# Optimization experiments

Hardware: AMD Instinct MI355X
Metric: run time of the kernel (lower is better)

Reference implementation:

```python
import jax, jax.numpy as jnp
import numpy as np

N_EMBD = 384
NUM_HEADS = 6
HEAD_SIZE = 64


def setup_inputs() -> dict:
    key = jax.random.key(0)
    ks = jax.random.split(key, 6)
    B, T = 128, 256
    D = NUM_HEADS * HEAD_SIZE  # 384
    x = jax.random.normal(ks[0], (B, T, N_EMBD), dtype=jnp.float32)
    Wk = jax.random.normal(ks[1], (N_EMBD, D), dtype=jnp.float32) * (N_EMBD ** -0.5)
    Wq = jax.random.normal(ks[2], (N_EMBD, D), dtype=jnp.float32) * (N_EMBD ** -0.5)
    Wv = jax.random.normal(ks[3], (N_EMBD, D), dtype=jnp.float32) * (N_EMBD ** -0.5)
    Wp = jax.random.normal(ks[4], (D, N_EMBD), dtype=jnp.float32) * (D ** -0.5)
    bp = jax.random.normal(ks[5], (N_EMBD,), dtype=jnp.float32) * 0.01
    return {"x": x, "Wk": Wk, "Wq": Wq, "Wv": Wv, "Wp": Wp, "bp": bp}


def reference(x, Wk, Wq, Wv, Wp, bp):
    B, T, C = x.shape
    H, hs = NUM_HEADS, HEAD_SIZE
    # QKV projections -> [B, H, T, hs]
    q = (x @ Wq).reshape(B, T, H, hs).transpose(0, 2, 1, 3)
    k = (x @ Wk).reshape(B, T, H, hs).transpose(0, 2, 1, 3)
    v = (x @ Wv).reshape(B, T, H, hs).transpose(0, 2, 1, 3)
    # NOTE: original scales by C**-0.5 where C = n_embd (not head_size)
    scale = jnp.asarray(C, x.dtype) ** -0.5
    wei = jnp.einsum('bhtd,bhsd->bhts', q, k) * scale  # [B, H, T, T]
    causal = jnp.tril(jnp.ones((T, T), dtype=bool))
    wei = jnp.where(causal, wei, -jnp.inf)
    wei = jax.nn.softmax(wei, axis=-1)
    # dropout disabled (eval mode) for deterministic reference
    out = jnp.einsum('bhts,bhsd->bhtd', wei, v)  # [B, H, T, hs]
    out = out.transpose(0, 2, 1, 3).reshape(B, T, H * hs)
    return out @ Wp + bp
```

## Files before the change

### kernel.cpp

```cpp
#include <hip/hip_runtime.h>
#include <hip/hip_bf16.h>


#define T_SEQ 256
#define NH 6
#define HS 64
#define CIN 384
#define BATCH 128
#define BT (BATCH * T_SEQ)
#define ELEMS ((size_t)BT * CIN)

using f32x4  = __attribute__((ext_vector_type(4))) float;
using bf16x8 = __attribute__((ext_vector_type(8))) short;

typedef __attribute__((address_space(3))) void       lds_vp;
typedef __attribute__((address_space(1))) const void glob_vp;

static __device__ __forceinline__ unsigned short f2bf(float f) {
  union { float f; unsigned u; } v; v.f = f;
  unsigned r = v.u + 0x7FFFu + ((v.u >> 16) & 1u);
  return (unsigned short)(r >> 16);
}

static __device__ __forceinline__ bf16x8 ld_bf8(const unsigned short* p) {
  return *reinterpret_cast<const bf16x8*>(p);
}

static __device__ __forceinline__ void gl_lds16(const void* g, void* l) {
  __builtin_amdgcn_global_load_lds((glob_vp*)g, (lds_vp*)l, 16, 0, 0);
}

__global__ __launch_bounds__(256) void convert_x(
    const float* __restrict__ x, unsigned short* __restrict__ xb)
{
  size_t i = (((size_t)blockIdx.x << 8) + threadIdx.x) << 3;
  float4 f0 = *reinterpret_cast<const float4*>(x + i);
  float4 f1 = *reinterpret_cast<const float4*>(x + i + 4);
  uint4 pk;
  pk.x = f2bf(f0.x) | ((unsigned)f2bf(f0.y) << 16);
  pk.y = f2bf(f0.z) | ((unsigned)f2bf(f0.w) << 16);
  pk.z = f2bf(f1.x) | ((unsigned)f2bf(f1.y) << 16);
  pk.w = f2bf(f1.z) | ((unsigned)f2bf(f1.w) << 16);
  *reinterpret_cast<uint4*>(xb + i) = pk;
}

__global__ __launch_bounds__(256) void convert_wqkv(
    const float* __restrict__ Wq, const float* __restrict__ Wk,
    const float* __restrict__ Wv, unsigned short* __restrict__ dst)
{
  __shared__ float t[32][33];
  const int z = blockIdx.z;
  const float* __restrict__ W = (z == 0) ? Wq : (z == 1) ? Wk : Wv;
  const int tx = threadIdx.x & 31, ty = threadIdx.x >> 5;
  const int k0 = blockIdx.x * 32, n0 = blockIdx.y * 32;
#pragma unroll
  for (int i = 0; i < 4; ++i)
    t[ty + 8 * i][tx] = W[(size_t)(k0 + ty + 8 * i) * CIN + n0 + tx];
  __syncthreads();
#pragma unroll
  for (int i = 0; i < 4; ++i)
    dst[((size_t)z * CIN + n0 + ty + 8 * i) * CIN + k0 + tx] =
        f2bf(t[tx][ty + 8 * i]);
}

__global__ __launch_bounds__(256) void transpose_w(
    const float* __restrict__ W, unsigned short* __restrict__ dst)
{
  __shared__ float t[32][33];
  const int tx = threadIdx.x & 31, ty = threadIdx.x >> 5;
  const int k0 = blockIdx.x * 32, n0 = blockIdx.y * 32;
#pragma unroll
  for (int i = 0; i < 4; ++i)
    t[ty + 8 * i][tx] = W[(size_t)(k0 + ty + 8 * i) * CIN + n0 + tx];
  __syncthreads();
#pragma unroll
  for (int i = 0; i < 4; ++i)
    dst[((size_t)(n0 + ty + 8 * i)) * CIN + k0 + tx] = f2bf(t[tx][ty + 8 * i]);
}

__global__ __launch_bounds__(256) void gemm_qkv(
    const unsigned short* __restrict__ xb,
    const unsigned short* __restrict__ wt,
    unsigned short* __restrict__ q_ws, unsigned short* __restrict__ k_ws,
    unsigned short* __restrict__ vT_ws)
{
  __shared__ __align__(16) unsigned short SM[2][128][64];

  const int tid = threadIdx.x;
  const int w = tid >> 6, l = tid & 63, g = l >> 4, c = l & 15;
  const int wr = w >> 1, wc = w & 1;

  const int wid = ((int)blockIdx.x & 7) * 288 + ((int)blockIdx.x >> 3);
  const int n_t = wid % 9, m_t = wid / 9;
  const int m0 = m_t * 128, n0 = n_t * 128;

  f32x4 acc[4][4];
#pragma unroll
  for (int mi = 0; mi < 4; ++mi)
#pragma unroll
    for (int nj = 0; nj < 4; ++nj) { f32x4 zz = {0.f,0.f,0.f,0.f}; acc[mi][nj] = zz; }

  const int lrow = l >> 3;
  const int lchk = (l & 7) ^ lrow;
  const char* ga = (const char*)xb +
      ((size_t)(m0 + w * 32 + lrow) * CIN + lchk * 8) * 2;
  const char* gb = (const char*)wt +
      ((size_t)(n0 + w * 32 + lrow) * CIN + lchk * 8) * 2;

  for (int t = 0; t < 6; ++t) {
#pragma unroll
    for (int i_ = 0; i_ < 4; ++i_) {
      gl_lds16(ga + (t * 64 + i_ * 8 * CIN) * 2, &SM[0][w * 32 + i_ * 8][0]);
      gl_lds16(gb + (t * 64 + i_ * 8 * CIN) * 2, &SM[1][w * 32 + i_ * 8][0]);
    }
    __syncthreads();
#pragma unroll
    for (int kk = 0; kk < 2; ++kk) {
      bf16x8 a[4], b[4];
#pragma unroll
      for (int mi = 0; mi < 4; ++mi) {
        const int row = wr * 64 + mi * 16 + c;
        a[mi] = *reinterpret_cast<const bf16x8*>(
            (const char*)&SM[0][row][0] + (((kk * 4 + g) ^ (c & 7)) << 4));
      }
#pragma unroll
      for (int nj = 0; nj < 4; ++nj) {
        const int row = wc * 64 + nj * 16 + c;
        b[nj] = *reinterpret_cast<const bf16x8*>(
            (const char*)&SM[1][row][0] + (((kk * 4 + g) ^ (c & 7)) << 4));
      }
      __builtin_amdgcn_s_setprio(1);
#pragma unroll
      for (int mi = 0; mi < 4; ++mi)
#pragma unroll
        for (int nj = 0; nj < 4; ++nj)
          acc[mi][nj] = __builtin_amdgcn_mfma_f32_16x16x32_bf16(
              a[mi], b[nj], acc[mi][nj], 0, 0, 0);
      __builtin_amdgcn_s_setprio(0);
    }
    __syncthreads();
  }

  const int z = n_t / 3;
  const int colw = (n_t % 3) * 128 + wc * 64;
  const int h = colw >> 6;
  const int b = m0 >> 8;
  const int trow0 = (m0 & 255) + wr * 64;

  if (z == 2) {
#pragma unroll
    for (int nj = 0; nj < 4; ++nj) {
      const int d = nj * 16 + c;
#pragma unroll
      for (int mi = 0; mi < 4; ++mi) {
        const int t0 = trow0 + mi * 16 + 4 * g;
        ushort4 pk;
        pk.x = f2bf(acc[mi][nj][0]); pk.y = f2bf(acc[mi][nj][1]);
        pk.z = f2bf(acc[mi][nj][2]); pk.w = f2bf(acc[mi][nj][3]);
        *reinterpret_cast<ushort4*>(
            vT_ws + (((size_t)b * NH + h) * HS + d) * T_SEQ + t0) = pk;
      }
    }
  } else {
    unsigned short* dstb = (z == 0) ? q_ws : k_ws;
    char* OS = (char*)SM + w * 8192;
#pragma unroll
    for (int nj = 0; nj < 4; ++nj)
#pragma unroll
      for (int mi = 0; mi < 4; ++mi)
#pragma unroll
        for (int i = 0; i < 4; ++i) {
          const int r = mi * 16 + 4 * g + i;
          const int chk = (nj * 2 + (c >> 3)) ^ (r & 7);
          *reinterpret_cast<unsigned short*>(
              OS + r * 128 + (chk << 4) + (c & 7) * 2) = f2bf(acc[mi][nj][i]);
        }
    __syncthreads();
    unsigned short* gdst = dstb + (((size_t)b * NH + h) * T_SEQ + trow0) * HS;
#pragma unroll
    for (int p = 0; p < 8; ++p) {
      const int r = p * 8 + (l >> 3);
      const int chk = (l & 7) ^ (r & 7);
      uint4 v = *reinterpret_cast<const uint4*>(OS + r * 128 + (chk << 4));
      *reinterpret_cast<uint4*>((char*)gdst + r * 128 + (l & 7) * 16) = v;
    }
  }
}

template<int NT>
__device__ __forceinline__ void attn_tile(
    const unsigned short* __restrict__ qg,
    const unsigned short* KL, const unsigned short* VL,
    unsigned short* __restrict__ o_ws, int bh, int qt, int g, int c)
{
  const int q0 = qt * 16;
  const int kxor = (c & 7) << 4;

  const char* qrow = (const char*)qg + (size_t)(q0 + c) * 128;
  const bf16x8 qb0 = *reinterpret_cast<const bf16x8*>(qrow + g * 16);
  const bf16x8 qb1 = *reinterpret_cast<const bf16x8*>(qrow + 64 + g * 16);

  f32x4 s[NT];
#pragma unroll
  for (int kt = 0; kt < NT; ++kt) {
    const char* krow = (const char*)KL + (kt * 16 + c) * 128;
    bf16x8 ka0 = *reinterpret_cast<const bf16x8*>(krow + ((g * 16) ^ kxor));
    bf16x8 ka1 = *reinterpret_cast<const bf16x8*>(krow + ((64 + g * 16) ^ kxor));
    f32x4 z = {0.f, 0.f, 0.f, 0.f};
    __builtin_amdgcn_s_setprio(1);
    z = __builtin_amdgcn_mfma_f32_16x16x32_bf16(ka0, qb0, z, 0, 0, 0);
    z = __builtin_amdgcn_mfma_f32_16x16x32_bf16(ka1, qb1, z, 0, 0, 0);
    __builtin_amdgcn_s_setprio(0);
    s[kt] = z;
  }

  const float sc = 0.07362372251839260f;
  float mx = -1e30f;
#pragma unroll
  for (int kt = 0; kt < NT; ++kt)
#pragma unroll
    for (int i = 0; i < 4; ++i) {
      const int k = kt * 16 + 4 * g + i;
      float v = (k <= q0 + c) ? s[kt][i] * sc : -1e30f;
      s[kt][i] = v;
      mx = fmaxf(mx, v);
    }
  mx = fmaxf(mx, __shfl_xor(mx, 16));
  mx = fmaxf(mx, __shfl_xor(mx, 32));

  float sum = 0.f;
#pragma unroll
  for (int kt = 0; kt < NT; ++kt)
#pragma unroll
    for (int i = 0; i < 4; ++i) {
      float p = __builtin_exp2f(s[kt][i] - mx);
      s[kt][i] = p;
      sum += p;
    }
  sum += __shfl_xor(sum, 16);
  sum += __shfl_xor(sum, 32);
  const float inv = 1.0f / sum;

  unsigned pk0[NT], pk1[NT];
#pragma unroll
  for (int kt = 0; kt < NT; ++kt) {
    float2 p01 = {s[kt][0] * inv, s[kt][1] * inv};
    float2 p23 = {s[kt][2] * inv, s[kt][3] * inv};
    __hip_bfloat162 b01 = __float22bfloat162_rn(p01);
    __hip_bfloat162 b23 = __float22bfloat162_rn(p23);
    pk0[kt] = *reinterpret_cast<unsigned*>(&b01);
    pk1[kt] = *reinterpret_cast<unsigned*>(&b23);
  }

  f32x4 acc[4];
#pragma unroll
  for (int nt = 0; nt < 4; ++nt) { f32x4 zz = {0.f,0.f,0.f,0.f}; acc[nt] = zz; }

  const int srcA = ((g & 1) << 5) + c;
  const int srcB = srcA + 16;
  const bool hi = (g >= 2);
#pragma unroll
  for (int ks = 0; ks < NT / 2; ++ks) {
    unsigned a0A = __shfl(pk0[2 * ks],     srcA);
    unsigned a1A = __shfl(pk1[2 * ks],     srcA);
    unsigned a0B = __shfl(pk0[2 * ks],     srcB);
    unsigned a1B = __shfl(pk1[2 * ks],     srcB);
    unsigned b0A = __shfl(pk0[2 * ks + 1], srcA);
    unsigned b1A = __shfl(pk1[2 * ks + 1], srcA);
    unsigned b0B = __shfl(pk0[2 * ks + 1], srcB);
    unsigned b1B = __shfl(pk1[2 * ks + 1], srcB);
    union { unsigned u[4]; bf16x8 v; } pa;
    pa.u[0] = hi ? b0A : a0A;
    pa.u[1] = hi ? b1A : a1A;
    pa.u[2] = hi ? b0B : a0B;
    pa.u[3] = hi ? b1B : a1B;
    __builtin_amdgcn_s_setprio(1);
#pragma unroll
    for (int nt = 0; nt < 4; ++nt) {
      const char* vrow = (const char*)VL + (nt * 16 + c) * 512;
      bf16x8 vb = *reinterpret_cast<const bf16x8*>(
          vrow + ((ks * 64 + g * 16) ^ kxor));
      acc[nt] = __builtin_amdgcn_mfma_f32_16x16x32_bf16(pa.v, vb, acc[nt], 0, 0, 0);
    }
    __builtin_amdgcn_s_setprio(0);
  }

  const int b = bh / NH, h = bh % NH;
  unsigned short* ob = o_ws + ((size_t)(b * T_SEQ + q0)) * CIN + h * HS;
#pragma unroll
  for (int nt = 0; nt < 4; ++nt)
#pragma unroll
    for (int i = 0; i < 4; ++i)
      ob[(size_t)(4 * g + i) * CIN + nt * 16 + c] = f2bf(acc[nt][i]);
}

__global__ __launch_bounds__(512, 4) void attn_kernel(
    const unsigned short* __restrict__ q_ws,
    const unsigned short* __restrict__ k_ws,
    const unsigned short* __restrict__ vT_ws,
    unsigned short* __restrict__ o_ws)
{
  __shared__ __align__(16) unsigned short KL[256 * 64];
  __shared__ __align__(16) unsigned short VL[64 * 256];

  const int tid = threadIdx.x;
  const int w = tid >> 6, l = tid & 63, g = l >> 4, c = l & 15;
  const int bh = blockIdx.x;

  const char* kg = (const char*)(k_ws + (size_t)bh * T_SEQ * HS);
  const char* vg = (const char*)(vT_ws + (size_t)bh * HS * T_SEQ);
#pragma unroll
  for (int i = 0; i < 4; ++i) {
    const int cid = i * 512 + w * 64 + l;
    const int rk = cid >> 3, pk_ = cid & 7;
    gl_lds16(kg + rk * 128 + ((pk_ ^ (rk & 7)) << 4),
             (char*)KL + (size_t)(i * 512 + w * 64) * 16);
    const int rv = cid >> 5, pv = cid & 31;
    const int sv = (pv & ~7) | ((pv & 7) ^ (rv & 7));
    gl_lds16(vg + rv * 512 + (sv << 4),
             (char*)VL + (size_t)(i * 512 + w * 64) * 16);
  }
  __syncthreads();

  const unsigned short* qg = q_ws + (size_t)bh * T_SEQ * HS;
  switch (w) {
    case 0: attn_tile<2>(qg, KL, VL, o_ws, bh, 0, g, c);
            attn_tile<16>(qg, KL, VL, o_ws, bh, 15, g, c); break;
    case 1: attn_tile<2>(qg, KL, VL, o_ws, bh, 1, g, c);
            attn_tile<16>(qg, KL, VL, o_ws, bh, 14, g, c); break;
    case 2: attn_tile<4>(qg, KL, VL, o_ws, bh, 2, g, c);
            attn_tile<14>(qg, KL, VL, o_ws, bh, 13, g, c); break;
    case 3: attn_tile<4>(qg, KL, VL, o_ws, bh, 3, g, c);
            attn_tile<14>(qg, KL, VL, o_ws, bh, 12, g, c); break;
    case 4: attn_tile<6>(qg, KL, VL, o_ws, bh, 4, g, c);
            attn_tile<12>(qg, KL, VL, o_ws, bh, 11, g, c); break;
    case 5: attn_tile<6>(qg, KL, VL, o_ws, bh, 5, g, c);
            attn_tile<12>(qg, KL, VL, o_ws, bh, 10, g, c); break;
    case 6: attn_tile<8>(qg, KL, VL, o_ws, bh, 6, g, c);
            attn_tile<10>(qg, KL, VL, o_ws, bh, 9, g, c); break;
    case 7: attn_tile<8>(qg, KL, VL, o_ws, bh, 7, g, c);
            attn_tile<10>(qg, KL, VL, o_ws, bh, 8, g, c); break;
  }
}

__global__ __launch_bounds__(256) void proj_kernel(
    const unsigned short* __restrict__ ob,
    const unsigned short* __restrict__ wpt,
    const float* __restrict__ bp,
    float* __restrict__ out)
{
  __shared__ __align__(16) unsigned short SM[2][128][64];

  const int tid = threadIdx.x;
  const int w = tid >> 6, l = tid & 63, g = l >> 4, c = l & 15;
  const int wr = w >> 1, wc = w & 1;

  const int wid = ((int)blockIdx.x & 7) * 96 + ((int)blockIdx.x >> 3);
  const int n_t = wid % 3, m_t = wid / 3;
  const int m0 = m_t * 128, n0 = n_t * 128;

  f32x4 acc[4][4];
#pragma unroll
  for (int mi = 0; mi < 4; ++mi)
#pragma unroll
    for (int nj = 0; nj < 4; ++nj) { f32x4 zz = {0.f,0.f,0.f,0.f}; acc[mi][nj] = zz; }

  const int lrow = l >> 3;
  const int lchk = (l & 7) ^ lrow;
  const char* ga = (const char*)ob +
      ((size_t)(m0 + w * 32 + lrow) * CIN + lchk * 8) * 2;
  const char* gb = (const char*)wpt +
      ((size_t)(n0 + w * 32 + lrow) * CIN + lchk * 8) * 2;

  for (int t = 0; t < 6; ++t) {
#pragma unroll
    for (int i_ = 0; i_ < 4; ++i_) {
      gl_lds16(ga + (t * 64 + i_ * 8 * CIN) * 2, &SM[0][w * 32 + i_ * 8][0]);
      gl_lds16(gb + (t * 64 + i_ * 8 * CIN) * 2, &SM[1][w * 32 + i_ * 8][0]);
    }
    __syncthreads();
#pragma unroll
    for (int kk = 0; kk < 2; ++kk) {
      bf16x8 a[4], b[4];
#pragma unroll
      for (int mi = 0; mi < 4; ++mi) {
        const int row = wr * 64 + mi * 16 + c;
        a[mi] = *reinterpret_cast<const bf16x8*>(
            (const char*)&SM[0][row][0] + (((kk * 4 + g) ^ (c & 7)) << 4));
      }
#pragma unroll
      for (int nj = 0; nj < 4; ++nj) {
        const int row = wc * 64 + nj * 16 + c;
        b[nj] = *reinterpret_cast<const bf16x8*>(
            (const char*)&SM[1][row][0] + (((kk * 4 + g) ^ (c & 7)) << 4));
      }
      __builtin_amdgcn_s_setprio(1);
#pragma unroll
      for (int mi = 0; mi < 4; ++mi)
#pragma unroll
        for (int nj = 0; nj < 4; ++nj)
          acc[mi][nj] = __builtin_amdgcn_mfma_f32_16x16x32_bf16(
              a[mi], b[nj], acc[mi][nj], 0, 0, 0);
      __builtin_amdgcn_s_setprio(0);
    }
    __syncthreads();
  }

#pragma unroll
  for (int nj = 0; nj < 4; ++nj) {
    const int col = n0 + wc * 64 + nj * 16 + c;
    const float bias = bp[col];
#pragma unroll
    for (int mi = 0; mi < 4; ++mi) {
      const int mrow = m0 + wr * 64 + mi * 16 + 4 * g;
#pragma unroll
      for (int i = 0; i < 4; ++i)
        out[(size_t)(mrow + i) * CIN + col] = acc[mi][nj][i] + bias;
    }
  }
}

extern "C" void kernel_launch(void* const* d_in, const int* in_sizes, int n_in,
                              void* d_out, int out_size, void* d_ws, size_t ws_size,
                              hipStream_t stream)
{
  const float* x  = (const float*)d_in[0];
  const float* Wk = (const float*)d_in[1];
  const float* Wq = (const float*)d_in[2];
  const float* Wv = (const float*)d_in[3];
  const float* Wp = (const float*)d_in[4];
  const float* bp = (const float*)d_in[5];
  float* out = (float*)d_out;

  unsigned short* ws    = (unsigned short*)d_ws;
  unsigned short* xb_o  = ws;
  unsigned short* q_ws  = ws + ELEMS;
  unsigned short* k_ws  = ws + 2 * ELEMS;
  unsigned short* vT_ws = ws + 3 * ELEMS;
  unsigned short* wqkvT = (unsigned short*)d_out;

  convert_x   <<<6144, 256, 0, stream>>>(x, xb_o);
  convert_wqkv<<<dim3(12, 12, 3), 256, 0, stream>>>(Wq, Wk, Wv, wqkvT);
  gemm_qkv    <<<2304, 256, 0, stream>>>(xb_o, wqkvT, q_ws, k_ws, vT_ws);
  attn_kernel <<<BATCH * NH, 512, 0, stream>>>(q_ws, k_ws, vT_ws, xb_o);
  transpose_w <<<dim3(12, 12), 256, 0, stream>>>(Wp, q_ws);
  proj_kernel <<<768, 256, 0, stream>>>(xb_o, q_ws, bp, out);
}
```

Baseline: 115.8 us.

## Grow QKV and projection GEMM tiles to 256x128 with 512-thread blocks

Both GEMM kernels now use 8 waves per block and a 256-row M tile that shares one 128-column B tile. This halves the redundant loads of weight tiles per output and halves the grid size. The QKV epilogue is split into two passes through LDS so the staging fits in the smaller A buffer. The risk is fewer blocks and lower occupancy, plus extra barriers in the epilogue.

```diff
diff --git a/kernel.cpp b/kernel.cpp
--- a/kernel.cpp
+++ b/kernel.cpp
@@ -20,10 +20,6 @@
   union { float f; unsigned u; } v; v.f = f;
   unsigned r = v.u + 0x7FFFu + ((v.u >> 16) & 1u);
   return (unsigned short)(r >> 16);
-}
-
-static __device__ __forceinline__ bf16x8 ld_bf8(const unsigned short* p) {
-  return *reinterpret_cast<const bf16x8*>(p);
 }
 
 static __device__ __forceinline__ void gl_lds16(const void* g, void* l) {
@@ -78,21 +74,22 @@
     dst[((size_t)(n0 + ty + 8 * i)) * CIN + k0 + tx] = f2bf(t[tx][ty + 8 * i]);
 }
 
-__global__ __launch_bounds__(256) void gemm_qkv(
+__global__ __launch_bounds__(512) void gemm_qkv(
     const unsigned short* __restrict__ xb,
     const unsigned short* __restrict__ wt,
     unsigned short* __restrict__ q_ws, unsigned short* __restrict__ k_ws,
     unsigned short* __restrict__ vT_ws)
 {
-  __shared__ __align__(16) unsigned short SM[2][128][64];
+  __shared__ __align__(16) unsigned short A [256][64];
+  __shared__ __align__(16) unsigned short Bt[128][64];
 
   const int tid = threadIdx.x;
   const int w = tid >> 6, l = tid & 63, g = l >> 4, c = l & 15;
   const int wr = w >> 1, wc = w & 1;
 
-  const int wid = ((int)blockIdx.x & 7) * 288 + ((int)blockIdx.x >> 3);
+  const int wid = ((int)blockIdx.x & 7) * 144 + ((int)blockIdx.x >> 3);
   const int n_t = wid % 9, m_t = wid / 9;
-  const int m0 = m_t * 128, n0 = n_t * 128;
+  const int m0 = m_t * 256, n0 = n_t * 128;
 
   f32x4 acc[4][4];
 #pragma unroll
@@ -100,19 +97,20 @@
 #pragma unroll
     for (int nj = 0; nj < 4; ++nj) { f32x4 zz = {0.f,0.f,0.f,0.f}; acc[mi][nj] = zz; }
 
-  const int lrow = l >> 3;
-  const int lchk = (l & 7) ^ lrow;
+  const int lr = l >> 3;
+  const int cc = (l & 7) ^ lr;
   const char* ga = (const char*)xb +
-      ((size_t)(m0 + w * 32 + lrow) * CIN + lchk * 8) * 2;
+      ((size_t)(m0 + w * 32 + lr) * CIN + (cc << 3)) * 2;
   const char* gb = (const char*)wt +
-      ((size_t)(n0 + w * 32 + lrow) * CIN + lchk * 8) * 2;
+      ((size_t)(n0 + w * 16 + lr) * CIN + (cc << 3)) * 2;
 
   for (int t = 0; t < 6; ++t) {
 #pragma unroll
-    for (int i_ = 0; i_ < 4; ++i_) {
-      gl_lds16(ga + (t * 64 + i_ * 8 * CIN) * 2, &SM[0][w * 32 + i_ * 8][0]);
-      gl_lds16(gb + (t * 64 + i_ * 8 * CIN) * 2, &SM[1][w * 32 + i_ * 8][0]);
-    }
+    for (int i_ = 0; i_ < 4; ++i_)
+      gl_lds16(ga + (t * 64 + i_ * 8 * CIN) * 2, &A[w * 32 + i_ * 8][0]);
+#pragma unroll
+    for (int i_ = 0; i_ < 2; ++i_)
+      gl_lds16(gb + (t * 64 + i_ * 8 * CIN) * 2, &Bt[w * 16 + i_ * 8][0]);
     __syncthreads();
 #pragma unroll
     for (int kk = 0; kk < 2; ++kk) {
@@ -121,13 +119,13 @@
       for (int mi = 0; mi < 4; ++mi) {
         const int row = wr * 64 + mi * 16 + c;
         a[mi] = *reinterpret_cast<const bf16x8*>(
-            (const char*)&SM[0][row][0] + (((kk * 4 + g) ^ (c & 7)) << 4));
+            (const char*)&A[row][0] + (((kk * 4 + g) ^ (c & 7)) << 4));
       }
 #pragma unroll
       for (int nj = 0; nj < 4; ++nj) {
         const int row = wc * 64 + nj * 16 + c;
         b[nj] = *reinterpret_cast<const bf16x8*>(
-            (const char*)&SM[1][row][0] + (((kk * 4 + g) ^ (c & 7)) << 4));
+            (const char*)&Bt[row][0] + (((kk * 4 + g) ^ (c & 7)) << 4));
       }
       __builtin_amdgcn_s_setprio(1);
 #pragma unroll
@@ -142,10 +140,9 @@
   }
 
   const int z = n_t / 3;
-  const int colw = (n_t % 3) * 128 + wc * 64;
-  const int h = colw >> 6;
-  const int b = m0 >> 8;
-  const int trow0 = (m0 & 255) + wr * 64;
+  const int h = ((n_t % 3) * 128 + wc * 64) >> 6;
+  const int b = m_t;
+  const int trow0 = wr * 64;
 
   if (z == 2) {
 #pragma unroll
@@ -163,26 +160,32 @@
     }
   } else {
     unsigned short* dstb = (z == 0) ? q_ws : k_ws;
-    char* OS = (char*)SM + w * 8192;
-#pragma unroll
-    for (int nj = 0; nj < 4; ++nj)
-#pragma unroll
-      for (int mi = 0; mi < 4; ++mi)
-#pragma unroll
-        for (int i = 0; i < 4; ++i) {
-          const int r = mi * 16 + 4 * g + i;
-          const int chk = (nj * 2 + (c >> 3)) ^ (r & 7);
-          *reinterpret_cast<unsigned short*>(
-              OS + r * 128 + (chk << 4) + (c & 7) * 2) = f2bf(acc[mi][nj][i]);
-        }
-    __syncthreads();
+    char* OS = (char*)A + w * 4096;
     unsigned short* gdst = dstb + (((size_t)b * NH + h) * T_SEQ + trow0) * HS;
 #pragma unroll
-    for (int p = 0; p < 8; ++p) {
-      const int r = p * 8 + (l >> 3);
-      const int chk = (l & 7) ^ (r & 7);
-      uint4 v = *reinterpret_cast<const uint4*>(OS + r * 128 + (chk << 4));
-      *reinterpret_cast<uint4*>((char*)gdst + r * 128 + (l & 7) * 16) = v;
+    for (int p = 0; p < 2; ++p) {
+#pragma unroll
+      for (int nj = 0; nj < 4; ++nj)
+#pragma unroll
+        for (int mi2 = 0; mi2 < 2; ++mi2)
+#pragma unroll
+          for (int i = 0; i < 4; ++i) {
+            const int r = mi2 * 16 + 4 * g + i;
+            const int chk = (nj * 2 + (c >> 3)) ^ (r & 7);
+            *reinterpret_cast<unsigned short*>(
+                OS + r * 128 + (chk << 4) + (c & 7) * 2) =
+                f2bf(acc[p * 2 + mi2][nj][i]);
+          }
+      __syncthreads();
+#pragma unroll
+      for (int i2 = 0; i2 < 4; ++i2) {
+        const int r = i2 * 8 + (l >> 3);
+        const int chk = (l & 7) ^ (r & 7);
+        uint4 v = *reinterpret_cast<const uint4*>(OS + r * 128 + (chk << 4));
+        *reinterpret_cast<uint4*>(
+            (char*)gdst + (p * 32 + r) * 128 + (l & 7) * 16) = v;
+      }
+      __syncthreads();
     }
   }
 }
@@ -343,21 +346,22 @@
   }
 }
 
-__global__ __launch_bounds__(256) void proj_kernel(
+__global__ __launch_bounds__(512) void proj_kernel(
     const unsigned short* __restrict__ ob,
     const unsigned short* __restrict__ wpt,
     const float* __restrict__ bp,
     float* __restrict__ out)
 {
-  __shared__ __align__(16) unsigned short SM[2][128][64];
+  __shared__ __align__(16) unsigned short A [256][64];
+  __shared__ __align__(16) unsigned short Bt[128][64];
 
   const int tid = threadIdx.x;
   const int w = tid >> 6, l = tid & 63, g = l >> 4, c = l & 15;
   const int wr = w >> 1, wc = w & 1;
 
-  const int wid = ((int)blockIdx.x & 7) * 96 + ((int)blockIdx.x >> 3);
+  const int wid = ((int)blockIdx.x & 7) * 48 + ((int)blockIdx.x >> 3);
   const int n_t = wid % 3, m_t = wid / 3;
-  const int m0 = m_t * 128, n0 = n_t * 128;
+  const int m0 = m_t * 256, n0 = n_t * 128;
 
   f32x4 acc[4][4];
 #pragma unroll
@@ -365,19 +369,20 @@
 #pragma unroll
     for (int nj = 0; nj < 4; ++nj) { f32x4 zz = {0.f,0.f,0.f,0.f}; acc[mi][nj] = zz; }
 
-  const int lrow = l >> 3;
-  const int lchk = (l & 7) ^ lrow;
+  const int lr = l >> 3;
+  const int cc = (l & 7) ^ lr;
   const char* ga = (const char*)ob +
-      ((size_t)(m0 + w * 32 + lrow) * CIN + lchk * 8) * 2;
+      ((size_t)(m0 + w * 32 + lr) * CIN + (cc << 3)) * 2;
   const char* gb = (const char*)wpt +
-      ((size_t)(n0 + w * 32 + lrow) * CIN + lchk * 8) * 2;
+      ((size_t)(n0 + w * 16 + lr) * CIN + (cc << 3)) * 2;
 
   for (int t = 0; t < 6; ++t) {
 #pragma unroll
-    for (int i_ = 0; i_ < 4; ++i_) {
-      gl_lds16(ga + (t * 64 + i_ * 8 * CIN) * 2, &SM[0][w * 32 + i_ * 8][0]);
-      gl_lds16(gb + (t * 64 + i_ * 8 * CIN) * 2, &SM[1][w * 32 + i_ * 8][0]);
-    }
+    for (int i_ = 0; i_ < 4; ++i_)
+      gl_lds16(ga + (t * 64 + i_ * 8 * CIN) * 2, &A[w * 32 + i_ * 8][0]);
+#pragma unroll
+    for (int i_ = 0; i_ < 2; ++i_)
+      gl_lds16(gb + (t * 64 + i_ * 8 * CIN) * 2, &Bt[w * 16 + i_ * 8][0]);
     __syncthreads();
 #pragma unroll
     for (int kk = 0; kk < 2; ++kk) {
@@ -386,13 +391,13 @@
       for (int mi = 0; mi < 4; ++mi) {
         const int row = wr * 64 + mi * 16 + c;
         a[mi] = *reinterpret_cast<const bf16x8*>(
-            (const char*)&SM[0][row][0] + (((kk * 4 + g) ^ (c & 7)) << 4));
+            (const char*)&A[row][0] + (((kk * 4 + g) ^ (c & 7)) << 4));
       }
 #pragma unroll
       for (int nj = 0; nj < 4; ++nj) {
         const int row = wc * 64 + nj * 16 + c;
         b[nj] = *reinterpret_cast<const bf16x8*>(
-            (const char*)&SM[1][row][0] + (((kk * 4 + g) ^ (c & 7)) << 4));
+            (const char*)&Bt[row][0] + (((kk * 4 + g) ^ (c & 7)) << 4));
       }
       __builtin_amdgcn_s_setprio(1);
 #pragma unroll
@@ -441,8 +446,8 @@
 
   convert_x   <<<6144, 256, 0, stream>>>(x, xb_o);
   convert_wqkv<<<dim3(12, 12, 3), 256, 0, stream>>>(Wq, Wk, Wv, wqkvT);
-  gemm_qkv    <<<2304, 256, 0, stream>>>(xb_o, wqkvT, q_ws, k_ws, vT_ws);
+  gemm_qkv    <<<1152, 512, 0, stream>>>(xb_o, wqkvT, q_ws, k_ws, vT_ws);
   attn_kernel <<<BATCH * NH, 512, 0, stream>>>(q_ws, k_ws, vT_ws, xb_o);
   transpose_w <<<dim3(12, 12), 256, 0, stream>>>(Wp, q_ws);
-  proj_kernel <<<768, 256, 0, stream>>>(xb_o, q_ws, bp, out);
-}
+  proj_kernel <<<384, 512, 0, stream>>>(xb_o, q_ws, bp, out);
+}
```

New measurement: 119.5 us. 3.2% more time.

## Fuse QKV projection into attention kernel, computing K/V straight into LDS

Applied to the files above, without the earlier changes.

Removes the separate QKV GEMM kernel and its Q/K/V workspace round-trip. Each attention block (one batch-head) now computes its own K and V tiles with MFMA from bf16 x and weights, writes them swizzled into shared memory, and keeps Q in registers, redistributing it via shuffles into MFMA operand layout. This saves the HBM write and read of Q, K and V. In exchange it re-reads x once per head, streams weights from global memory without LDS staging, and uses more registers.

```diff
diff --git a/kernel.cpp b/kernel.cpp
--- a/kernel.cpp
+++ b/kernel.cpp
@@ -78,127 +78,48 @@
     dst[((size_t)(n0 + ty + 8 * i)) * CIN + k0 + tx] = f2bf(t[tx][ty + 8 * i]);
 }
 
-__global__ __launch_bounds__(256) void gemm_qkv(
-    const unsigned short* __restrict__ xb,
-    const unsigned short* __restrict__ wt,
-    unsigned short* __restrict__ q_ws, unsigned short* __restrict__ k_ws,
-    unsigned short* __restrict__ vT_ws)
-{
-  __shared__ __align__(16) unsigned short SM[2][128][64];
-
-  const int tid = threadIdx.x;
-  const int w = tid >> 6, l = tid & 63, g = l >> 4, c = l & 15;
-  const int wr = w >> 1, wc = w & 1;
-
-  const int wid = ((int)blockIdx.x & 7) * 288 + ((int)blockIdx.x >> 3);
-  const int n_t = wid % 9, m_t = wid / 9;
-  const int m0 = m_t * 128, n0 = n_t * 128;
-
-  f32x4 acc[4][4];
-#pragma unroll
-  for (int mi = 0; mi < 4; ++mi)
-#pragma unroll
-    for (int nj = 0; nj < 4; ++nj) { f32x4 zz = {0.f,0.f,0.f,0.f}; acc[mi][nj] = zz; }
-
-  const int lrow = l >> 3;
-  const int lchk = (l & 7) ^ lrow;
-  const char* ga = (const char*)xb +
-      ((size_t)(m0 + w * 32 + lrow) * CIN + lchk * 8) * 2;
-  const char* gb = (const char*)wt +
-      ((size_t)(n0 + w * 32 + lrow) * CIN + lchk * 8) * 2;
-
-  for (int t = 0; t < 6; ++t) {
-#pragma unroll
-    for (int i_ = 0; i_ < 4; ++i_) {
-      gl_lds16(ga + (t * 64 + i_ * 8 * CIN) * 2, &SM[0][w * 32 + i_ * 8][0]);
-      gl_lds16(gb + (t * 64 + i_ * 8 * CIN) * 2, &SM[1][w * 32 + i_ * 8][0]);
-    }
-    __syncthreads();
-#pragma unroll
-    for (int kk = 0; kk < 2; ++kk) {
-      bf16x8 a[4], b[4];
-#pragma unroll
-      for (int mi = 0; mi < 4; ++mi) {
-        const int row = wr * 64 + mi * 16 + c;
-        a[mi] = *reinterpret_cast<const bf16x8*>(
-            (const char*)&SM[0][row][0] + (((kk * 4 + g) ^ (c & 7)) << 4));
-      }
-#pragma unroll
-      for (int nj = 0; nj < 4; ++nj) {
-        const int row = wc * 64 + nj * 16 + c;
-        b[nj] = *reinterpret_cast<const bf16x8*>(
-            (const char*)&SM[1][row][0] + (((kk * 4 + g) ^ (c & 7)) << 4));
-      }
-      __builtin_amdgcn_s_setprio(1);
-#pragma unroll
-      for (int mi = 0; mi < 4; ++mi)
-#pragma unroll
-        for (int nj = 0; nj < 4; ++nj)
-          acc[mi][nj] = __builtin_amdgcn_mfma_f32_16x16x32_bf16(
-              a[mi], b[nj], acc[mi][nj], 0, 0, 0);
-      __builtin_amdgcn_s_setprio(0);
-    }
-    __syncthreads();
-  }
-
-  const int z = n_t / 3;
-  const int colw = (n_t % 3) * 128 + wc * 64;
-  const int h = colw >> 6;
-  const int b = m0 >> 8;
-  const int trow0 = (m0 & 255) + wr * 64;
-
-  if (z == 2) {
-#pragma unroll
-    for (int nj = 0; nj < 4; ++nj) {
-      const int d = nj * 16 + c;
-#pragma unroll
-      for (int mi = 0; mi < 4; ++mi) {
-        const int t0 = trow0 + mi * 16 + 4 * g;
-        ushort4 pk;
-        pk.x = f2bf(acc[mi][nj][0]); pk.y = f2bf(acc[mi][nj][1]);
-        pk.z = f2bf(acc[mi][nj][2]); pk.w = f2bf(acc[mi][nj][3]);
-        *reinterpret_cast<ushort4*>(
-            vT_ws + (((size_t)b * NH + h) * HS + d) * T_SEQ + t0) = pk;
-      }
-    }
-  } else {
-    unsigned short* dstb = (z == 0) ? q_ws : k_ws;
-    char* OS = (char*)SM + w * 8192;
-#pragma unroll
-    for (int nj = 0; nj < 4; ++nj)
-#pragma unroll
-      for (int mi = 0; mi < 4; ++mi)
-#pragma unroll
-        for (int i = 0; i < 4; ++i) {
-          const int r = mi * 16 + 4 * g + i;
-          const int chk = (nj * 2 + (c >> 3)) ^ (r & 7);
-          *reinterpret_cast<unsigned short*>(
-              OS + r * 128 + (chk << 4) + (c & 7) * 2) = f2bf(acc[mi][nj][i]);
-        }
-    __syncthreads();
-    unsigned short* gdst = dstb + (((size_t)b * NH + h) * T_SEQ + trow0) * HS;
-#pragma unroll
-    for (int p = 0; p < 8; ++p) {
-      const int r = p * 8 + (l >> 3);
-      const int chk = (l & 7) ^ (r & 7);
-      uint4 v = *reinterpret_cast<const uint4*>(OS + r * 128 + (chk << 4));
-      *reinterpret_cast<uint4*>((char*)gdst + r * 128 + (l & 7) * 16) = v;
-    }
-  }
-}
 
 template<int NT>
-__device__ __forceinline__ void attn_tile(
-    const unsigned short* __restrict__ qg,
+__device__ __forceinline__ void attn_run(
+    f32x4 aq0, f32x4 aq1, f32x4 aq2, f32x4 aq3,
     const unsigned short* KL, const unsigned short* VL,
-    unsigned short* __restrict__ o_ws, int bh, int qt, int g, int c)
+    unsigned short* __restrict__ o_ws, int b, int h, int qt, int g, int c)
 {
   const int q0 = qt * 16;
   const int kxor = (c & 7) << 4;
 
-  const char* qrow = (const char*)qg + (size_t)(q0 + c) * 128;
-  const bf16x8 qb0 = *reinterpret_cast<const bf16x8*>(qrow + g * 16);
-  const bf16x8 qb1 = *reinterpret_cast<const bf16x8*>(qrow + 64 + g * 16);
+  f32x4 aqv[4] = {aq0, aq1, aq2, aq3};
+  unsigned pk0q[4], pk1q[4];
+#pragma unroll
+  for (int dt = 0; dt < 4; ++dt) {
+    float2 p01 = {aqv[dt][0], aqv[dt][1]};
+    float2 p23 = {aqv[dt][2], aqv[dt][3]};
+    __hip_bfloat162 b01 = __float22bfloat162_rn(p01);
+    __hip_bfloat162 b23 = __float22bfloat162_rn(p23);
+    pk0q[dt] = *reinterpret_cast<unsigned*>(&b01);
+    pk1q[dt] = *reinterpret_cast<unsigned*>(&b23);
+  }
+  const int srcA = ((g & 1) << 5) + c;
+  const int srcB = srcA + 16;
+  const bool hi = (g >= 2);
+  union { unsigned u[4]; bf16x8 v; } qbu[2];
+#pragma unroll
+  for (int ks = 0; ks < 2; ++ks) {
+    unsigned a0A = __shfl(pk0q[2 * ks],     srcA);
+    unsigned a1A = __shfl(pk1q[2 * ks],     srcA);
+    unsigned a0B = __shfl(pk0q[2 * ks],     srcB);
+    unsigned a1B = __shfl(pk1q[2 * ks],     srcB);
+    unsigned b0A = __shfl(pk0q[2 * ks + 1], srcA);
+    unsigned b1A = __shfl(pk1q[2 * ks + 1], srcA);
+    unsigned b0B = __shfl(pk0q[2 * ks + 1], srcB);
+    unsigned b1B = __shfl(pk1q[2 * ks + 1], srcB);
+    qbu[ks].u[0] = hi ? b0A : a0A;
+    qbu[ks].u[1] = hi ? b1A : a1A;
+    qbu[ks].u[2] = hi ? b0B : a0B;
+    qbu[ks].u[3] = hi ? b1B : a1B;
+  }
+  const bf16x8 qb0 = qbu[0].v;
+  const bf16x8 qb1 = qbu[1].v;
 
   f32x4 s[NT];
 #pragma unroll
@@ -255,10 +176,6 @@
   f32x4 acc[4];
 #pragma unroll
   for (int nt = 0; nt < 4; ++nt) { f32x4 zz = {0.f,0.f,0.f,0.f}; acc[nt] = zz; }
-
-  const int srcA = ((g & 1) << 5) + c;
-  const int srcB = srcA + 16;
-  const bool hi = (g >= 2);
 #pragma unroll
   for (int ks = 0; ks < NT / 2; ++ks) {
     unsigned a0A = __shfl(pk0[2 * ks],     srcA);
@@ -285,7 +202,6 @@
     __builtin_amdgcn_s_setprio(0);
   }
 
-  const int b = bh / NH, h = bh % NH;
   unsigned short* ob = o_ws + ((size_t)(b * T_SEQ + q0)) * CIN + h * HS;
 #pragma unroll
   for (int nt = 0; nt < 4; ++nt)
@@ -294,10 +210,9 @@
       ob[(size_t)(4 * g + i) * CIN + nt * 16 + c] = f2bf(acc[nt][i]);
 }
 
-__global__ __launch_bounds__(512, 4) void attn_kernel(
-    const unsigned short* __restrict__ q_ws,
-    const unsigned short* __restrict__ k_ws,
-    const unsigned short* __restrict__ vT_ws,
+__global__ __launch_bounds__(512, 4) void fused_qkv_attn(
+    const unsigned short* __restrict__ xb,
+    const unsigned short* __restrict__ wt,
     unsigned short* __restrict__ o_ws)
 {
   __shared__ __align__(16) unsigned short KL[256 * 64];
@@ -305,41 +220,105 @@
 
   const int tid = threadIdx.x;
   const int w = tid >> 6, l = tid & 63, g = l >> 4, c = l & 15;
-  const int bh = blockIdx.x;
-
-  const char* kg = (const char*)(k_ws + (size_t)bh * T_SEQ * HS);
-  const char* vg = (const char*)(vT_ws + (size_t)bh * HS * T_SEQ);
-#pragma unroll
-  for (int i = 0; i < 4; ++i) {
-    const int cid = i * 512 + w * 64 + l;
-    const int rk = cid >> 3, pk_ = cid & 7;
-    gl_lds16(kg + rk * 128 + ((pk_ ^ (rk & 7)) << 4),
-             (char*)KL + (size_t)(i * 512 + w * 64) * 16);
-    const int rv = cid >> 5, pv = cid & 31;
-    const int sv = (pv & ~7) | ((pv & 7) ^ (rv & 7));
-    gl_lds16(vg + rv * 512 + (sv << 4),
-             (char*)VL + (size_t)(i * 512 + w * 64) * 16);
+  const int bh = ((int)blockIdx.x & 7) * 96 + ((int)blockIdx.x >> 3);
+  const int b = bh / NH, h = bh % NH;
+
+  const int tb0 = w * 16;
+  const int tb1 = (15 - w) * 16;
+
+  const unsigned short* xr0 = xb + ((size_t)(b * T_SEQ + tb0 + c)) * CIN + 8 * g;
+  const unsigned short* xr1 = xb + ((size_t)(b * T_SEQ + tb1 + c)) * CIN + 8 * g;
+  const unsigned short* wqr = wt + ((size_t)(h * HS + c)) * CIN + 8 * g;
+  const unsigned short* wkr = wt + ((size_t)(CIN + h * HS + c)) * CIN + 8 * g;
+  const unsigned short* wvr = wt + ((size_t)(2 * CIN + h * HS + c)) * CIN + 8 * g;
+
+  f32x4 ak[2][4], av[2][4];
+#pragma unroll
+  for (int t2 = 0; t2 < 2; ++t2)
+#pragma unroll
+    for (int dt = 0; dt < 4; ++dt) {
+      f32x4 zz = {0.f, 0.f, 0.f, 0.f};
+      ak[t2][dt] = zz; av[t2][dt] = zz;
+    }
+#pragma unroll 4
+  for (int ks2 = 0; ks2 < 12; ++ks2) {
+    const int ko = ks2 * 32;
+    bf16x8 xf0 = ld_bf8(xr0 + ko);
+    bf16x8 xf1 = ld_bf8(xr1 + ko);
+#pragma unroll
+    for (int dt = 0; dt < 4; ++dt) {
+      bf16x8 wkf = ld_bf8(wkr + dt * 16 * CIN + ko);
+      ak[0][dt] = __builtin_amdgcn_mfma_f32_16x16x32_bf16(wkf, xf0, ak[0][dt], 0, 0, 0);
+      ak[1][dt] = __builtin_amdgcn_mfma_f32_16x16x32_bf16(wkf, xf1, ak[1][dt], 0, 0, 0);
+      bf16x8 wvf = ld_bf8(wvr + dt * 16 * CIN + ko);
+      av[0][dt] = __builtin_amdgcn_mfma_f32_16x16x32_bf16(xf0, wvf, av[0][dt], 0, 0, 0);
+      av[1][dt] = __builtin_amdgcn_mfma_f32_16x16x32_bf16(xf1, wvf, av[1][dt], 0, 0, 0);
+    }
+  }
+
+#pragma unroll
+  for (int t2 = 0; t2 < 2; ++t2) {
+    const int trow = (t2 ? tb1 : tb0) + c;
+#pragma unroll
+    for (int dt = 0; dt < 4; ++dt) {
+      const int d0 = dt * 16 + 4 * g;
+      ushort4 pk;
+      pk.x = f2bf(ak[t2][dt][0]); pk.y = f2bf(ak[t2][dt][1]);
+      pk.z = f2bf(ak[t2][dt][2]); pk.w = f2bf(ak[t2][dt][3]);
+      const int byte = trow * 128 + (((d0 >> 3) ^ (trow & 7)) << 4) + (d0 & 7) * 2;
+      *reinterpret_cast<ushort4*>((char*)KL + byte) = pk;
+    }
+  }
+#pragma unroll
+  for (int t2 = 0; t2 < 2; ++t2) {
+    const int t0 = (t2 ? tb1 : tb0) + 4 * g;
+#pragma unroll
+    for (int nt = 0; nt < 4; ++nt) {
+      const int d = nt * 16 + c;
+      ushort4 pk;
+      pk.x = f2bf(av[t2][nt][0]); pk.y = f2bf(av[t2][nt][1]);
+      pk.z = f2bf(av[t2][nt][2]); pk.w = f2bf(av[t2][nt][3]);
+      const int byte = d * 512 + (((t0 >> 3) ^ (d & 7)) << 4) + (t0 & 7) * 2;
+      *reinterpret_cast<ushort4*>((char*)VL + byte) = pk;
+    }
+  }
+
+  f32x4 aq[2][4];
+#pragma unroll
+  for (int t2 = 0; t2 < 2; ++t2)
+#pragma unroll
+    for (int dt = 0; dt < 4; ++dt) { f32x4 zz = {0.f,0.f,0.f,0.f}; aq[t2][dt] = zz; }
+#pragma unroll 4
+  for (int ks2 = 0; ks2 < 12; ++ks2) {
+    const int ko = ks2 * 32;
+    bf16x8 xf0 = ld_bf8(xr0 + ko);
+    bf16x8 xf1 = ld_bf8(xr1 + ko);
+#pragma unroll
+    for (int dt = 0; dt < 4; ++dt) {
+      bf16x8 wqf = ld_bf8(wqr + dt * 16 * CIN + ko);
+      aq[0][dt] = __builtin_amdgcn_mfma_f32_16x16x32_bf16(wqf, xf0, aq[0][dt], 0, 0, 0);
+      aq[1][dt] = __builtin_amdgcn_mfma_f32_16x16x32_bf16(wqf, xf1, aq[1][dt], 0, 0, 0);
+    }
   }
   __syncthreads();
 
-  const unsigned short* qg = q_ws + (size_t)bh * T_SEQ * HS;
   switch (w) {
-    case 0: attn_tile<2>(qg, KL, VL, o_ws, bh, 0, g, c);
-            attn_tile<16>(qg, KL, VL, o_ws, bh, 15, g, c); break;
-    case 1: attn_tile<2>(qg, KL, VL, o_ws, bh, 1, g, c);
-            attn_tile<16>(qg, KL, VL, o_ws, bh, 14, g, c); break;
-    case 2: attn_tile<4>(qg, KL, VL, o_ws, bh, 2, g, c);
-            attn_tile<14>(qg, KL, VL, o_ws, bh, 13, g, c); break;
-    case 3: attn_tile<4>(qg, KL, VL, o_ws, bh, 3, g, c);
-            attn_tile<14>(qg, KL, VL, o_ws, bh, 12, g, c); break;
-    case 4: attn_tile<6>(qg, KL, VL, o_ws, bh, 4, g, c);
-            attn_tile<12>(qg, KL, VL, o_ws, bh, 11, g, c); break;
-    case 5: attn_tile<6>(qg, KL, VL, o_ws, bh, 5, g, c);
-            attn_tile<12>(qg, KL, VL, o_ws, bh, 10, g, c); break;
-    case 6: attn_tile<8>(qg, KL, VL, o_ws, bh, 6, g, c);
-            attn_tile<10>(qg, KL, VL, o_ws, bh, 9, g, c); break;
-    case 7: attn_tile<8>(qg, KL, VL, o_ws, bh, 7, g, c);
-            attn_tile<10>(qg, KL, VL, o_ws, bh, 8, g, c); break;
+    case 0: attn_run<2> (aq[0][0],aq[0][1],aq[0][2],aq[0][3], KL, VL, o_ws, b, h, 0,  g, c);
+            attn_run<16>(aq[1][0],aq[1][1],aq[1][2],aq[1][3], KL, VL, o_ws, b, h, 15, g, c); break;
+    case 1: attn_run<2> (aq[0][0],aq[0][1],aq[0][2],aq[0][3], KL, VL, o_ws, b, h, 1,  g, c);
+            attn_run<16>(aq[1][0],aq[1][1],aq[1][2],aq[1][3], KL, VL, o_ws, b, h, 14, g, c); break;
+    case 2: attn_run<4> (aq[0][0],aq[0][1],aq[0][2],aq[0][3], KL, VL, o_ws, b, h, 2,  g, c);
+            attn_run<14>(aq[1][0],aq[1][1],aq[1][2],aq[1][3], KL, VL, o_ws, b, h, 13, g, c); break;
+    case 3: attn_run<4> (aq[0][0],aq[0][1],aq[0][2],aq[0][3], KL, VL, o_ws, b, h, 3,  g, c);
+            attn_run<14>(aq[1][0],aq[1][1],aq[1][2],aq[1][3], KL, VL, o_ws, b, h, 12, g, c); break;
+    case 4: attn_run<6> (aq[0][0],aq[0][1],aq[0][2],aq[0][3], KL, VL, o_ws, b, h, 4,  g, c);
+            attn_run<12>(aq[1][0],aq[1][1],aq[1][2],aq[1][3], KL, VL, o_ws, b, h, 11, g, c); break;
+    case 5: attn_run<6> (aq[0][0],aq[0][1],aq[0][2],aq[0][3], KL, VL, o_ws, b, h, 5,  g, c);
+            attn_run<12>(aq[1][0],aq[1][1],aq[1][2],aq[1][3], KL, VL, o_ws, b, h, 10, g, c); break;
+    case 6: attn_run<8> (aq[0][0],aq[0][1],aq[0][2],aq[0][3], KL, VL, o_ws, b, h, 6,  g, c);
+            attn_run<10>(aq[1][0],aq[1][1],aq[1][2],aq[1][3], KL, VL, o_ws, b, h, 9,  g, c); break;
+    case 7: attn_run<8> (aq[0][0],aq[0][1],aq[0][2],aq[0][3], KL, VL, o_ws, b, h, 7,  g, c);
+            attn_run<10>(aq[1][0],aq[1][1],aq[1][2],aq[1][3], KL, VL, o_ws, b, h, 8,  g, c); break;
   }
 }
 
@@ -365,12 +344,12 @@
 #pragma unroll
     for (int nj = 0; nj < 4; ++nj) { f32x4 zz = {0.f,0.f,0.f,0.f}; acc[mi][nj] = zz; }
 
-  const int lrow = l >> 3;
-  const int lchk = (l & 7) ^ lrow;
+  const int lr = l >> 3;
+  const int cc = (l & 7) ^ lr;
   const char* ga = (const char*)ob +
-      ((size_t)(m0 + w * 32 + lrow) * CIN + lchk * 8) * 2;
+      ((size_t)(m0 + w * 32 + lr) * CIN + (cc << 3)) * 2;
   const char* gb = (const char*)wpt +
-      ((size_t)(n0 + w * 32 + lrow) * CIN + lchk * 8) * 2;
+      ((size_t)(n0 + w * 32 + lr) * CIN + (cc << 3)) * 2;
 
   for (int t = 0; t < 6; ++t) {
 #pragma unroll
@@ -433,16 +412,14 @@
   float* out = (float*)d_out;
 
   unsigned short* ws    = (unsigned short*)d_ws;
-  unsigned short* xb_o  = ws;
-  unsigned short* q_ws  = ws + ELEMS;
-  unsigned short* k_ws  = ws + 2 * ELEMS;
-  unsigned short* vT_ws = ws + 3 * ELEMS;
-  unsigned short* wqkvT = (unsigned short*)d_out;
-
-  convert_x   <<<6144, 256, 0, stream>>>(x, xb_o);
-  convert_wqkv<<<dim3(12, 12, 3), 256, 0, stream>>>(Wq, Wk, Wv, wqkvT);
-  gemm_qkv    <<<2304, 256, 0, stream>>>(xb_o, wqkvT, q_ws, k_ws, vT_ws);
-  attn_kernel <<<BATCH * NH, 512, 0, stream>>>(q_ws, k_ws, vT_ws, xb_o);
-  transpose_w <<<dim3(12, 12), 256, 0, stream>>>(Wp, q_ws);
-  proj_kernel <<<768, 256, 0, stream>>>(xb_o, q_ws, bp, out);
-}
+  unsigned short* xb    = ws;
+  unsigned short* o_ws  = ws + ELEMS;
+  unsigned short* wqkvT = ws + 2 * ELEMS;
+  unsigned short* wpT   = ws + 2 * ELEMS + (size_t)3 * CIN * CIN;
+
+  convert_x     <<<6144, 256, 0, stream>>>(x, xb);
+  convert_wqkv  <<<dim3(12, 12, 3), 256, 0, stream>>>(Wq, Wk, Wv, wqkvT);
+  transpose_w   <<<dim3(12, 12), 256, 0, stream>>>(Wp, wpT);
+  fused_qkv_attn<<<BATCH * NH, 512, 0, stream>>>(xb, wqkvT, o_ws);
+  proj_kernel   <<<768, 256, 0, stream>>>(o_ws, wpT, bp, out);
+}
```

New measurement: 191.1 us. +65.0%, slower.
